# Kernel optimization log

Hardware: AMD Instinct MI355X
Metric: run time of the kernel (lower is better)

## Reference

```python
import jax, jax.numpy as jnp
import numpy as np

B, N, D, Z, H = 256, 128, 256, 64, 128

def setup_inputs() -> dict:
    key = jax.random.key(0)
    ks = jax.random.split(key, 12)
    s = 0.02
    inp = {
        "h_obs": jax.random.normal(ks[0], (B, N, D), jnp.float32),
        "z": jax.random.normal(ks[1], (B, N, Z), jnp.float32),
        "start_pos": jax.random.normal(ks[2], (B, N, 2), jnp.float32),
        # input_proj: Linear(D+Z+2 -> H)
        "W_in": jax.random.normal(ks[3], (D + Z + 2, H), jnp.float32) * s,
        "b_in": jax.random.normal(ks[4], (H,), jnp.float32) * s,
        # GRUCell weights, PyTorch layout: [3H, H] rows ordered (r, z, n)
        "W_ih": jax.random.normal(ks[5], (3 * H, H), jnp.float32) * s,
        "b_ih": jax.random.normal(ks[6], (3 * H,), jnp.float32) * s,
        "W_hh": jax.random.normal(ks[7], (3 * H, H), jnp.float32) * s,
        "b_hh": jax.random.normal(ks[8], (3 * H,), jnp.float32) * s,
        # out_proj: Linear(H -> 2)
        "W_out": jax.random.normal(ks[9], (2, H), jnp.float32) * s,
        "b_out": jax.random.normal(ks[10], (2,), jnp.float32) * s,
        "pred_len": 30,
    }
    return inp

def _gru_cell(x, h, W_ih, b_ih, W_hh, b_hh):
    gi = x @ W_ih.T + b_ih            # [BN, 3H]
    gh = h @ W_hh.T + b_hh            # [BN, 3H]
    i_r, i_z, i_n = jnp.split(gi, 3, axis=-1)
    h_r, h_z, h_n = jnp.split(gh, 3, axis=-1)
    r = jax.nn.sigmoid(i_r + h_r)
    zg = jax.nn.sigmoid(i_z + h_z)
    n = jnp.tanh(i_n + r * h_n)
    return (1.0 - zg) * n + zg * h

def reference(h_obs, z, start_pos, W_in, b_in, W_ih, b_ih, W_hh, b_hh, W_out, b_out, pred_len):
    BN = B * N
    # h_obs and z are constant across steps: precompute their projection once.
    base = jnp.concatenate([h_obs, z], axis=-1).reshape(BN, D + Z)
    base_proj = base @ W_in[: D + Z] + b_in            # [BN, H]
    W_pos = W_in[D + Z:]                               # [2, H]

    state0 = jnp.zeros((BN, H), h_obs.dtype)
    pos0 = start_pos.reshape(BN, 2)

    def step(carry, _):
        state, pos = carry
        x = base_proj + pos @ W_pos                    # == input_proj(cat(h,z,pos))
        state = _gru_cell(x, state, W_ih, b_ih, W_hh, b_hh)
        delta = state @ W_out.T + b_out                # [BN, 2]
        pos = pos + delta
        return (state, pos), pos

    (_, _), traj = jax.lax.scan(step, (state0, pos0), None, length=pred_len)
    # traj: [T, BN, 2] -> [B, T, N, 2]
    return traj.reshape(pred_len, B, N, 2).transpose(1, 0, 2, 3)
```

## Files before the change

kernel.cpp:

```cpp
#include <hip/hip_runtime.h>
#include <hip/hip_bf16.h>


#define T_LEN 30
#define H_    128
#define G3_   384
#define KIN_  320
#define S_    152
#define HBYTES (64*S_*2)
#define TRAJ_OFF (2*HBYTES)
#define LDS_BYTES (TRAJ_OFF + T_LEN*64*2*4)

#define SCL_RZ -1.44269504088896341f
#define SCL_N   2.88539008177792681f

typedef float  f32x4 __attribute__((ext_vector_type(4)));
typedef __bf16 b16x8 __attribute__((ext_vector_type(8)));

#define MFMA16(a,b,c) __builtin_amdgcn_mfma_f32_16x16x32_bf16((a),(b),(c),0,0,0)

__device__ __forceinline__ b16x8 pack8s(const float* p, float s){
  b16x8 r;
  #pragma unroll
  for (int i=0;i<8;i++) r[i] = (__bf16)(s*p[i]);
  return r;
}

__global__ void prep_wc(const float* __restrict__ W_in, const float* __restrict__ W_ih,
                        __bf16* __restrict__ WcT){
  __shared__ float win[H_];
  int k = blockIdx.x;
  if (threadIdx.x < H_) win[threadIdx.x] = W_in[(size_t)k*H_ + threadIdx.x];
  __syncthreads();
  int j = threadIdx.x;
  const float* wr = W_ih + (size_t)j*H_;
  float s = 0.f;
  #pragma unroll 8
  for (int m=0;m<H_;m++) s += wr[m]*win[m];
  float scl = (j < 2*H_) ? SCL_RZ : SCL_N;
  WcT[(size_t)j*KIN_ + k] = (__bf16)(scl*s);
}

__global__ void prep_vec(const float* __restrict__ W_in, const float* __restrict__ b_in,
                         const float* __restrict__ W_ih, const float* __restrict__ b_ih,
                         const float* __restrict__ b_hh,
                         float* __restrict__ cvec, float* __restrict__ P2G){
  int j = threadIdx.x;
  const float* wr = W_ih + (size_t)j*H_;
  float s  = b_ih[j] + (j < 2*H_ ? b_hh[j] : 0.f);
  float p0 = 0.f, p1 = 0.f;
  #pragma unroll 8
  for (int m=0;m<H_;m++){
    float w = wr[m];
    s  += b_in[m]*w;
    p0 += W_in[(size_t)KIN_*H_ + m]*w;
    p1 += W_in[(size_t)(KIN_+1)*H_ + m]*w;
  }
  float scl = (j < 2*H_) ? SCL_RZ : SCL_N;
  cvec[j] = scl*s; P2G[j] = scl*p0; P2G[G3_ + j] = scl*p1;
}

__global__ __launch_bounds__(512, 2)
void decoder(const float* __restrict__ h_obs, const float* __restrict__ zin,
             const float* __restrict__ start_pos,
             const float* __restrict__ W_hh, const float* __restrict__ b_hh,
             const float* __restrict__ W_out, const float* __restrict__ b_out,
             const __bf16* __restrict__ WcT, const float* __restrict__ cvec,
             const float* __restrict__ P2G, float* __restrict__ out)
{
  __shared__ __align__(16) char lds[LDS_BYTES];
  __bf16* hbuf = (__bf16*)lds;
  float*  traj = (float*)(lds + TRAJ_OFF);
  __bf16* stg  = (__bf16*)lds;

  const int tid  = threadIdx.x;
  const int lane = tid & 63;
  const int w    = tid >> 6;
  const int l15  = lane & 15;
  const int lhi  = lane >> 4;
  const int R0   = blockIdx.x << 6;
  const int hcol = (w<<4) + l15;
  const int jr = hcol, jz = H_ + hcol, jn = 2*H_ + hcol;
  const int oc = l15 & 1;

  {
    const float4* src = reinterpret_cast<const float4*>(h_obs) + (size_t)R0*64;
    #pragma unroll
    for (int i=0;i<8;i++){
      int k = tid + (i<<9);
      float4 v = src[k];
      int r = k>>6, c = (k&63)<<2;
      __bf16* d = &stg[r*328 + c];
      d[0]=(__bf16)v.x; d[1]=(__bf16)v.y; d[2]=(__bf16)v.z; d[3]=(__bf16)v.w;
    }
    const float4* srcz = reinterpret_cast<const float4*>(zin) + (size_t)R0*16;
    #pragma unroll
    for (int i=0;i<2;i++){
      int k = tid + (i<<9);
      float4 v = srcz[k];
      int r = k>>4, c = 256 + ((k&15)<<2);
      __bf16* d = &stg[r*328 + c];
      d[0]=(__bf16)v.x; d[1]=(__bf16)v.y; d[2]=(__bf16)v.z; d[3]=(__bf16)v.w;
    }
  }
  __syncthreads();

  f32x4 G[2][3][2];
  {
    float cr = cvec[jr], cz = cvec[jz], cn = cvec[jn];
    #pragma unroll
    for (int g=0; g<2; g++){
      G[g][0][0] = (f32x4){cr,cr,cr,cr}; G[g][0][1] = G[g][0][0];
      G[g][1][0] = (f32x4){cz,cz,cz,cz}; G[g][1][1] = G[g][1][0];
      G[g][2][0] = (f32x4){cn,cn,cn,cn}; G[g][2][1] = G[g][2][0];
    }
    #pragma unroll 1
    for (int kk=0; kk<10; kk++){
      const int ko = (kk<<5) + (lhi<<3);
      b16x8 br = *reinterpret_cast<const b16x8*>(WcT + (size_t)jr*KIN_ + ko);
      b16x8 bz = *reinterpret_cast<const b16x8*>(WcT + (size_t)jz*KIN_ + ko);
      b16x8 bn = *reinterpret_cast<const b16x8*>(WcT + (size_t)jn*KIN_ + ko);
      #pragma unroll
      for (int g=0; g<2; g++){
        b16x8 a0 = *reinterpret_cast<const b16x8*>(&stg[(g*32   +l15)*328 + ko]);
        b16x8 a1 = *reinterpret_cast<const b16x8*>(&stg[(g*32+16+l15)*328 + ko]);
        G[g][0][0] = MFMA16(a0, br, G[g][0][0]); G[g][0][1] = MFMA16(a1, br, G[g][0][1]);
        G[g][1][0] = MFMA16(a0, bz, G[g][1][0]); G[g][1][1] = MFMA16(a1, bz, G[g][1][1]);
        G[g][2][0] = MFMA16(a0, bn, G[g][2][0]); G[g][2][1] = MFMA16(a1, bn, G[g][2][1]);
      }
    }
  }

  b16x8 Bh[3][4], Bo[4];
  #pragma unroll
  for (int kk=0;kk<4;kk++){
    const int ko = (kk<<5) + (lhi<<3);
    Bh[0][kk] = pack8s(W_hh + (size_t)jr*H_ + ko, SCL_RZ);
    Bh[1][kk] = pack8s(W_hh + (size_t)jz*H_ + ko, SCL_RZ);
    Bh[2][kk] = pack8s(W_hh + (size_t)jn*H_ + ko, SCL_N);
    Bo[kk]    = pack8s(W_out + (size_t)oc*H_ + ko, 1.0f);
  }
  const float pgr0 = P2G[jr], pgr1 = P2G[G3_+jr];
  const float pgz0 = P2G[jz], pgz1 = P2G[G3_+jz];
  const float pgn0 = P2G[jn], pgn1 = P2G[G3_+jn];
  const float bhn  = SCL_N * b_hh[2*H_ + hcol];
  const float bo   = b_out[oc];
  const f32x4 bovec  = (f32x4){bo,bo,bo,bo};
  const f32x4 bhnvec = (f32x4){bhn,bhn,bhn,bhn};

  float posx[2][2][4], posy[2][2][4], st[2][2][4];
  #pragma unroll
  for (int g=0; g<2; g++)
    #pragma unroll
    for (int m=0;m<2;m++)
      #pragma unroll
      for (int q=0;q<4;q++){
        int r = R0 + (g<<5) + (m<<4) + (lhi<<2) + q;
        posx[g][m][q] = start_pos[2*r];
        posy[g][m][q] = start_pos[2*r+1];
      }

  __syncthreads();

  #pragma unroll
  for (int g=0; g<2; g++)
    #pragma unroll
    for (int m=0;m<2;m++)
      #pragma unroll
      for (int q=0;q<4;q++){
        float p0 = posx[g][m][q], p1 = posy[g][m][q];
        float rg = __builtin_amdgcn_rcpf(1.f + __builtin_amdgcn_exp2f(
                     fmaf(p1,pgr1, fmaf(p0,pgr0, G[g][0][m][q]))));
        float zg = __builtin_amdgcn_rcpf(1.f + __builtin_amdgcn_exp2f(
                     fmaf(p1,pgz1, fmaf(p0,pgz0, G[g][1][m][q]))));
        float inn = fmaf(p1,pgn1, fmaf(p0,pgn0, G[g][2][m][q]));
        float nn = fmaf(-2.f, __builtin_amdgcn_rcpf(1.f + __builtin_amdgcn_exp2f(
                     fmaf(rg, bhn, inn))), 1.f);
        float hnew = nn - zg*nn;
        st[g][m][q] = hnew;
        hbuf[((g<<5)+(m<<4)+(lhi<<2)+q)*S_ + hcol] = (__bf16)hnew;
      }

  const unsigned rdbA = (unsigned)(l15*(S_*2) + (lhi<<4));
  const unsigned wrbA = (unsigned)((lhi<<2)*(S_*2) + hcol*2);

  int cur = 0;
  #pragma unroll 1
  for (int t=1; t<T_LEN; ++t){
    __syncthreads();
    const char* rb = lds + cur*HBYTES;
    char*       wb = lds + (cur^1)*HBYTES;

    #pragma unroll
    for (int g=0; g<2; g++){
      const unsigned go = g*(32*S_*2);
      f32x4 ar0, ar1, az0, az1, an0, an1, d0, d1;
      #pragma unroll
      for (int kk=0;kk<4;kk++){
        b16x8 a0 = *reinterpret_cast<const b16x8*>(rb + go + rdbA + kk*64);
        b16x8 a1 = *reinterpret_cast<const b16x8*>(rb + go + rdbA + 16*S_*2 + kk*64);
        if (kk==0){
          d0  = MFMA16(a0, Bo[0],   bovec);  d1  = MFMA16(a1, Bo[0],   bovec);
          ar0 = MFMA16(a0, Bh[0][0], G[g][0][0]); ar1 = MFMA16(a1, Bh[0][0], G[g][0][1]);
          az0 = MFMA16(a0, Bh[1][0], G[g][1][0]); az1 = MFMA16(a1, Bh[1][0], G[g][1][1]);
          an0 = MFMA16(a0, Bh[2][0], bhnvec);     an1 = MFMA16(a1, Bh[2][0], bhnvec);
        } else {
          d0  = MFMA16(a0, Bo[kk],   d0);  d1  = MFMA16(a1, Bo[kk],   d1);
          ar0 = MFMA16(a0, Bh[0][kk], ar0); ar1 = MFMA16(a1, Bh[0][kk], ar1);
          az0 = MFMA16(a0, Bh[1][kk], az0); az1 = MFMA16(a1, Bh[1][kk], az1);
          an0 = MFMA16(a0, Bh[2][kk], an0); an1 = MFMA16(a1, Bh[2][kk], an1);
        }
      }
      #pragma unroll
      for (int m=0;m<2;m++)
        #pragma unroll
        for (int q=0;q<4;q++){
          float dme  = (m==0)? d0[q] : d1[q];
          float doth = __shfl_xor(dme, 1);
          posx[g][m][q] += oc ? doth : dme;
          posy[g][m][q] += oc ? dme  : doth;
        }
      if (w==g && l15==0){
        #pragma unroll
        for (int m=0;m<2;m++)
          #pragma unroll
          for (int q=0;q<4;q++){
            int rr = (g<<5) + (m<<4) + (lhi<<2) + q;
            float2 v; v.x = posx[g][m][q]; v.y = posy[g][m][q];
            *reinterpret_cast<float2*>(&traj[(t-1)*128 + rr*2]) = v;
          }
      }
      #pragma unroll
      for (int m=0;m<2;m++)
        #pragma unroll
        for (int q=0;q<4;q++){
          float p0 = posx[g][m][q], p1 = posy[g][m][q];
          float ar = (m==0)? ar0[q] : ar1[q];
          float az = (m==0)? az0[q] : az1[q];
          float hn = (m==0)? an0[q] : an1[q];
          float rg = __builtin_amdgcn_rcpf(1.f + __builtin_amdgcn_exp2f(
                       fmaf(p1,pgr1, fmaf(p0,pgr0, ar))));
          float zg = __builtin_amdgcn_rcpf(1.f + __builtin_amdgcn_exp2f(
                       fmaf(p1,pgz1, fmaf(p0,pgz0, az))));
          float inn = fmaf(p1,pgn1, fmaf(p0,pgn0, G[g][2][m][q]));
          float nn = fmaf(-2.f, __builtin_amdgcn_rcpf(1.f + __builtin_amdgcn_exp2f(
                       fmaf(rg, hn, inn))), 1.f);
          float hnew = fmaf(zg, st[g][m][q] - nn, nn);
          st[g][m][q] = hnew;
          *reinterpret_cast<__bf16*>(wb + go + wrbA + (m*16+q)*(S_*2)) = (__bf16)hnew;
        }
    }
    cur ^= 1;
  }

  __syncthreads();
  {
    const char* rb = lds + cur*HBYTES;
    #pragma unroll
    for (int g=0; g<2; g++){
      const unsigned go = g*(32*S_*2);
      f32x4 d0, d1;
      #pragma unroll
      for (int kk=0;kk<4;kk++){
        b16x8 a0 = *reinterpret_cast<const b16x8*>(rb + go + rdbA + kk*64);
        b16x8 a1 = *reinterpret_cast<const b16x8*>(rb + go + rdbA + 16*S_*2 + kk*64);
        if (kk==0){ d0 = MFMA16(a0, Bo[0], bovec); d1 = MFMA16(a1, Bo[0], bovec); }
        else      { d0 = MFMA16(a0, Bo[kk], d0);   d1 = MFMA16(a1, Bo[kk], d1);   }
      }
      #pragma unroll
      for (int m=0;m<2;m++)
        #pragma unroll
        for (int q=0;q<4;q++){
          float dme  = (m==0)? d0[q] : d1[q];
          float doth = __shfl_xor(dme, 1);
          posx[g][m][q] += oc ? doth : dme;
          posy[g][m][q] += oc ? dme  : doth;
        }
      if (w==g && l15==0){
        #pragma unroll
        for (int m=0;m<2;m++)
          #pragma unroll
          for (int q=0;q<4;q++){
            int rr = (g<<5) + (m<<4) + (lhi<<2) + q;
            float2 v; v.x = posx[g][m][q]; v.y = posy[g][m][q];
            *reinterpret_cast<float2*>(&traj[(T_LEN-1)*128 + rr*2]) = v;
          }
      }
    }
  }

  __syncthreads();
  {
    const size_t ob  = ((size_t)(R0>>7)*T_LEN)<<8;
    const int    n02 = (R0 & 127)<<1;
    for (int i=tid; i<T_LEN*128; i+=512){
      int tt = i>>7, j = i&127;
      out[ob + (size_t)tt*256 + n02 + j] = traj[i];
    }
  }
}

extern "C" void kernel_launch(void* const* d_in, const int* in_sizes, int n_in,
                              void* d_out, int out_size, void* d_ws, size_t ws_size,
                              hipStream_t stream) {
  const float* h_obs     = (const float*)d_in[0];
  const float* z         = (const float*)d_in[1];
  const float* start_pos = (const float*)d_in[2];
  const float* W_in      = (const float*)d_in[3];
  const float* b_in      = (const float*)d_in[4];
  const float* W_ih      = (const float*)d_in[5];
  const float* b_ih      = (const float*)d_in[6];
  const float* W_hh      = (const float*)d_in[7];
  const float* b_hh      = (const float*)d_in[8];
  const float* W_out     = (const float*)d_in[9];
  const float* b_out     = (const float*)d_in[10];

  __bf16* WcT  = (__bf16*)d_ws;
  float*  cvec = (float*)((char*)d_ws + (size_t)G3_*KIN_*2);
  float*  P2G  = cvec + G3_;

  prep_wc <<<KIN_, G3_, 0, stream>>>(W_in, W_ih, WcT);
  prep_vec<<<1,    G3_, 0, stream>>>(W_in, b_in, W_ih, b_ih, b_hh, cvec, P2G);
  decoder <<<512, 512, 0, stream>>>(h_obs, z, start_pos, W_hh, b_hh, W_out, b_out,
                                    WcT, cvec, P2G, (float*)d_out);
}
```

Before: 309.8 us.

## Fold position feedback into recurrent GEMM weights and pack input gates to bf16

Position feedback is folded algebraically into the recurrent weights: a prep kernel builds augmented weights in which pos@W_pos is rewritten through W_out applied to the previous hidden state, plus a small K-extension MFMA carrying the current position stored in LDS. This removes the per-element FMA position terms from the gate math. The precomputed input-gate accumulators are stored as packed bf16 to free registers. Only four designated waves compute the output delta instead of every wave, and prep_wc is re-tiled to 16 outputs per block. The trade-offs are extra MFMAs per step, lower precision from bf16 rounding of the gate inputs and positions, and an additional prep launch.

```diff
diff --git a/kernel.cpp b/kernel.cpp
--- a/kernel.cpp
+++ b/kernel.cpp
@@ -6,16 +6,17 @@
 #define H_    128
 #define G3_   384
 #define KIN_  320
-#define S_    152
-#define HBYTES (64*S_*2)
-#define TRAJ_OFF (2*HBYTES)
-#define LDS_BYTES (TRAJ_OFF + T_LEN*64*2*4)
+#define S2B   336
+#define HB    (64*S2B)
+#define TRAJ_OFF (2*HB)
+#define LDS_BYTES (TRAJ_OFF + T_LEN*64*8)
 
 #define SCL_RZ -1.44269504088896341f
 #define SCL_N   2.88539008177792681f
 
 typedef float  f32x4 __attribute__((ext_vector_type(4)));
 typedef __bf16 b16x8 __attribute__((ext_vector_type(8)));
+typedef unsigned u32x4 __attribute__((ext_vector_type(4)));
 
 #define MFMA16(a,b,c) __builtin_amdgcn_mfma_f32_16x16x32_bf16((a),(b),(c),0,0,0)
 
@@ -25,25 +26,52 @@
   for (int i=0;i<8;i++) r[i] = (__bf16)(s*p[i]);
   return r;
 }
+__device__ __forceinline__ unsigned pk2(float a, float b){
+  __bf16 x=(__bf16)a, y=(__bf16)b;
+  unsigned short ux=__builtin_bit_cast(unsigned short,x);
+  unsigned short uy=__builtin_bit_cast(unsigned short,y);
+  return (unsigned)ux | ((unsigned)uy<<16);
+}
+__device__ __forceinline__ f32x4 unpk2(unsigned lo, unsigned hi){
+  f32x4 r;
+  r[0]=__builtin_bit_cast(float, lo<<16);
+  r[1]=__builtin_bit_cast(float, lo&0xFFFF0000u);
+  r[2]=__builtin_bit_cast(float, hi<<16);
+  r[3]=__builtin_bit_cast(float, hi&0xFFFF0000u);
+  return r;
+}
+__device__ __forceinline__ b16x8 fragu(unsigned v){
+  u32x4 t = {v,0u,0u,0u};
+  return __builtin_bit_cast(b16x8, t);
+}
 
 __global__ void prep_wc(const float* __restrict__ W_in, const float* __restrict__ W_ih,
                         __bf16* __restrict__ WcT){
-  __shared__ float win[H_];
-  int k = blockIdx.x;
-  if (threadIdx.x < H_) win[threadIdx.x] = W_in[(size_t)k*H_ + threadIdx.x];
+  __shared__ float win[H_][16];
+  int k0 = blockIdx.x << 4;
+  for (int i=threadIdx.x; i<16*H_; i+=384){
+    int kk = i>>7, m = i&127;
+    win[m][kk] = W_in[(size_t)(k0+kk)*H_ + m];
+  }
   __syncthreads();
   int j = threadIdx.x;
   const float* wr = W_ih + (size_t)j*H_;
-  float s = 0.f;
-  #pragma unroll 8
-  for (int m=0;m<H_;m++) s += wr[m]*win[m];
+  float acc[16];
+  #pragma unroll
+  for (int kk=0;kk<16;kk++) acc[kk]=0.f;
+  for (int m=0;m<H_;m++){
+    float wv = wr[m];
+    #pragma unroll
+    for (int kk=0;kk<16;kk++) acc[kk] = fmaf(wv, win[m][kk], acc[kk]);
+  }
   float scl = (j < 2*H_) ? SCL_RZ : SCL_N;
-  WcT[(size_t)j*KIN_ + k] = (__bf16)(scl*s);
+  #pragma unroll
+  for (int kk=0;kk<16;kk++) WcT[(size_t)j*KIN_ + k0 + kk] = (__bf16)(scl*acc[kk]);
 }
 
 __global__ void prep_vec(const float* __restrict__ W_in, const float* __restrict__ b_in,
                          const float* __restrict__ W_ih, const float* __restrict__ b_ih,
-                         const float* __restrict__ b_hh,
+                         const float* __restrict__ b_hh, const float* __restrict__ b_out,
                          float* __restrict__ cvec, float* __restrict__ P2G){
   int j = threadIdx.x;
   const float* wr = W_ih + (size_t)j*H_;
@@ -51,27 +79,45 @@
   float p0 = 0.f, p1 = 0.f;
   #pragma unroll 8
   for (int m=0;m<H_;m++){
-    float w = wr[m];
-    s  += b_in[m]*w;
-    p0 += W_in[(size_t)KIN_*H_ + m]*w;
-    p1 += W_in[(size_t)(KIN_+1)*H_ + m]*w;
+    float wv = wr[m];
+    s  += b_in[m]*wv;
+    p0 += W_in[(size_t)KIN_*H_ + m]*wv;
+    p1 += W_in[(size_t)(KIN_+1)*H_ + m]*wv;
   }
   float scl = (j < 2*H_) ? SCL_RZ : SCL_N;
-  cvec[j] = scl*s; P2G[j] = scl*p0; P2G[G3_ + j] = scl*p1;
+  float p0s = scl*p0, p1s = scl*p1;
+  P2G[j] = p0s; P2G[G3_ + j] = p1s;
+  cvec[j] = scl*s + b_out[0]*p0s + b_out[1]*p1s;
+}
+
+__global__ void prep_wt(const float* __restrict__ W_hh, const float* __restrict__ W_out,
+                        const float* __restrict__ P2G, __bf16* __restrict__ WT){
+  int jp = blockIdx.x;
+  int set = jp >> 7, col = jp & 127;
+  int j = (set==0) ? col : (set==1) ? H_+col : 2*H_+col;
+  float p0 = P2G[j], p1 = P2G[G3_+j];
+  int k = threadIdx.x;
+  if (k >= 136) return;
+  float v = 0.f;
+  if (k < 128){
+    if (set<=1)      v = SCL_RZ*W_hh[(size_t)j*H_+k] + p0*W_out[k] + p1*W_out[H_+k];
+    else if (set==2) v = SCL_N *W_hh[(size_t)j*H_+k];
+    else             v = p0*W_out[k] + p1*W_out[H_+k];
+  } else if (k==128){ v = (set==2)? 0.f : p0; }
+  else if (k==129){ v = (set==2)? 0.f : p1; }
+  WT[(size_t)jp*136 + k] = (__bf16)v;
 }
 
 __global__ __launch_bounds__(512, 2)
 void decoder(const float* __restrict__ h_obs, const float* __restrict__ zin,
              const float* __restrict__ start_pos,
-             const float* __restrict__ W_hh, const float* __restrict__ b_hh,
-             const float* __restrict__ W_out, const float* __restrict__ b_out,
+             const float* __restrict__ b_hh, const float* __restrict__ W_out,
+             const float* __restrict__ b_out,
              const __bf16* __restrict__ WcT, const float* __restrict__ cvec,
-             const float* __restrict__ P2G, float* __restrict__ out)
+             const __bf16* __restrict__ WT, float* __restrict__ out)
 {
   __shared__ __align__(16) char lds[LDS_BYTES];
-  __bf16* hbuf = (__bf16*)lds;
-  float*  traj = (float*)(lds + TRAJ_OFF);
-  __bf16* stg  = (__bf16*)lds;
+  __bf16* stg = (__bf16*)lds;
 
   const int tid  = threadIdx.x;
   const int lane = tid & 63;
@@ -82,6 +128,8 @@
   const int hcol = (w<<4) + l15;
   const int jr = hcol, jz = H_ + hcol, jn = 2*H_ + hcol;
   const int oc = l15 & 1;
+  const bool desig = (w < 4);
+  const int gd = w >> 1, md = w & 1;
 
   {
     const float4* src = reinterpret_cast<const float4*>(h_obs) + (size_t)R0*64;
@@ -103,10 +151,41 @@
       d[0]=(__bf16)v.x; d[1]=(__bf16)v.y; d[2]=(__bf16)v.z; d[3]=(__bf16)v.w;
     }
   }
+
+  const float bo0 = b_out[0], bo1 = b_out[1];
+  const float bo  = oc ? bo1 : bo0;
+  const float bhn = SCL_N * b_hh[2*H_ + hcol];
+  const f32x4 bhnvec = (f32x4){bhn,bhn,bhn,bhn};
+
+  b16x8 Br[4],Bz[4],Ban[4],Binn[4],Bo[4];
+  #pragma unroll
+  for (int kk=0;kk<4;kk++){
+    const int ko = kk*32 + lhi*8;
+    Br[kk]   = *reinterpret_cast<const b16x8*>(WT + (size_t)(      hcol)*136 + ko);
+    Bz[kk]   = *reinterpret_cast<const b16x8*>(WT + (size_t)(128 + hcol)*136 + ko);
+    Ban[kk]  = *reinterpret_cast<const b16x8*>(WT + (size_t)(256 + hcol)*136 + ko);
+    Binn[kk] = *reinterpret_cast<const b16x8*>(WT + (size_t)(384 + hcol)*136 + ko);
+    Bo[kk]   = pack8s(W_out + (size_t)oc*H_ + ko, 1.0f);
+  }
+  const b16x8 Br4 = fragu(lhi==0 ? *reinterpret_cast<const unsigned*>(WT + (size_t)(      hcol)*136 + 128) : 0u);
+  const b16x8 Bz4 = fragu(lhi==0 ? *reinterpret_cast<const unsigned*>(WT + (size_t)(128 + hcol)*136 + 128) : 0u);
+  const b16x8 Bi4 = fragu(lhi==0 ? *reinterpret_cast<const unsigned*>(WT + (size_t)(384 + hcol)*136 + 128) : 0u);
+
+  float px[4]={0,0,0,0}, py[4]={0,0,0,0};
+  if (desig){
+    #pragma unroll
+    for (int q=0;q<4;q++){
+      int r = R0 + gd*32 + md*16 + lhi*4 + q;
+      px[q] = start_pos[2*r]   - bo0;
+      py[q] = start_pos[2*r+1] - bo1;
+    }
+  }
+
   __syncthreads();
 
-  f32x4 G[2][3][2];
+  unsigned Gp[2][3][2][2];
   {
+    f32x4 G[2][3][2];
     float cr = cvec[jr], cz = cvec[jz], cn = cvec[jn];
     #pragma unroll
     for (int g=0; g<2; g++){
@@ -129,168 +208,170 @@
         G[g][2][0] = MFMA16(a0, bn, G[g][2][0]); G[g][2][1] = MFMA16(a1, bn, G[g][2][1]);
       }
     }
-  }
-
-  b16x8 Bh[3][4], Bo[4];
+    #pragma unroll
+    for (int g=0; g<2; g++)
+      #pragma unroll
+      for (int gate=0; gate<3; gate++)
+        #pragma unroll
+        for (int m=0; m<2; m++){
+          Gp[g][gate][m][0] = pk2(G[g][gate][m][0], G[g][gate][m][1]);
+          Gp[g][gate][m][1] = pk2(G[g][gate][m][2], G[g][gate][m][3]);
+        }
+  }
+  __syncthreads();
+
+  for (int i=tid; i<4096; i+=512){
+    int r = i>>6, wq = i&63;
+    *reinterpret_cast<unsigned*>(lds + r*S2B + wq*4) = 0u;
+  }
+  if (desig && l15==0){
+    #pragma unroll
+    for (int q=0;q<4;q++){
+      int row = gd*32 + md*16 + lhi*4 + q;
+      *reinterpret_cast<unsigned*>(lds + row*S2B + 256) = pk2(px[q], py[q]);
+    }
+  }
+
+  float st[2][2][4];
   #pragma unroll
-  for (int kk=0;kk<4;kk++){
-    const int ko = (kk<<5) + (lhi<<3);
-    Bh[0][kk] = pack8s(W_hh + (size_t)jr*H_ + ko, SCL_RZ);
-    Bh[1][kk] = pack8s(W_hh + (size_t)jz*H_ + ko, SCL_RZ);
-    Bh[2][kk] = pack8s(W_hh + (size_t)jn*H_ + ko, SCL_N);
-    Bo[kk]    = pack8s(W_out + (size_t)oc*H_ + ko, 1.0f);
-  }
-  const float pgr0 = P2G[jr], pgr1 = P2G[G3_+jr];
-  const float pgz0 = P2G[jz], pgz1 = P2G[G3_+jz];
-  const float pgn0 = P2G[jn], pgn1 = P2G[G3_+jn];
-  const float bhn  = SCL_N * b_hh[2*H_ + hcol];
-  const float bo   = b_out[oc];
-  const f32x4 bovec  = (f32x4){bo,bo,bo,bo};
-  const f32x4 bhnvec = (f32x4){bhn,bhn,bhn,bhn};
-
-  float posx[2][2][4], posy[2][2][4], st[2][2][4];
-  #pragma unroll
-  for (int g=0; g<2; g++)
+  for (int g=0;g<2;g++)
     #pragma unroll
     for (int m=0;m<2;m++)
       #pragma unroll
-      for (int q=0;q<4;q++){
-        int r = R0 + (g<<5) + (m<<4) + (lhi<<2) + q;
-        posx[g][m][q] = start_pos[2*r];
-        posy[g][m][q] = start_pos[2*r+1];
-      }
-
-  __syncthreads();
-
-  #pragma unroll
-  for (int g=0; g<2; g++)
-    #pragma unroll
-    for (int m=0;m<2;m++)
-      #pragma unroll
-      for (int q=0;q<4;q++){
-        float p0 = posx[g][m][q], p1 = posy[g][m][q];
-        float rg = __builtin_amdgcn_rcpf(1.f + __builtin_amdgcn_exp2f(
-                     fmaf(p1,pgr1, fmaf(p0,pgr0, G[g][0][m][q]))));
-        float zg = __builtin_amdgcn_rcpf(1.f + __builtin_amdgcn_exp2f(
-                     fmaf(p1,pgz1, fmaf(p0,pgz0, G[g][1][m][q]))));
-        float inn = fmaf(p1,pgn1, fmaf(p0,pgn0, G[g][2][m][q]));
-        float nn = fmaf(-2.f, __builtin_amdgcn_rcpf(1.f + __builtin_amdgcn_exp2f(
-                     fmaf(rg, bhn, inn))), 1.f);
-        float hnew = nn - zg*nn;
-        st[g][m][q] = hnew;
-        hbuf[((g<<5)+(m<<4)+(lhi<<2)+q)*S_ + hcol] = (__bf16)hnew;
-      }
-
-  const unsigned rdbA = (unsigned)(l15*(S_*2) + (lhi<<4));
-  const unsigned wrbA = (unsigned)((lhi<<2)*(S_*2) + hcol*2);
+      for (int q=0;q<4;q++) st[g][m][q] = 0.f;
+
+  const unsigned rdb = (unsigned)(l15*S2B + lhi*16);
+  const f32x4 zero4 = (f32x4){0,0,0,0};
 
   int cur = 0;
   #pragma unroll 1
-  for (int t=1; t<T_LEN; ++t){
+  for (int t=0; t<T_LEN; ++t){
     __syncthreads();
-    const char* rb = lds + cur*HBYTES;
-    char*       wb = lds + (cur^1)*HBYTES;
-
-    #pragma unroll
-    for (int g=0; g<2; g++){
-      const unsigned go = g*(32*S_*2);
-      f32x4 ar0, ar1, az0, az1, an0, an1, d0, d1;
+    const char* rb = lds + cur*HB;
+    char*       wb = lds + (cur^1)*HB;
+
+    #pragma unroll
+    for (int g=0; g<2; ++g){
+      const char* rg_ = rb + g*(32*S2B);
+      char*       wg_ = wb + g*(32*S2B);
+
+      f32x4 ar0 = unpk2(Gp[g][0][0][0], Gp[g][0][0][1]);
+      f32x4 ar1 = unpk2(Gp[g][0][1][0], Gp[g][0][1][1]);
+      f32x4 az0 = unpk2(Gp[g][1][0][0], Gp[g][1][0][1]);
+      f32x4 az1 = unpk2(Gp[g][1][1][0], Gp[g][1][1][1]);
+      f32x4 ai0 = unpk2(Gp[g][2][0][0], Gp[g][2][0][1]);
+      f32x4 ai1 = unpk2(Gp[g][2][1][0], Gp[g][2][1][1]);
+      f32x4 an0 = bhnvec, an1 = bhnvec;
+
       #pragma unroll
       for (int kk=0;kk<4;kk++){
-        b16x8 a0 = *reinterpret_cast<const b16x8*>(rb + go + rdbA + kk*64);
-        b16x8 a1 = *reinterpret_cast<const b16x8*>(rb + go + rdbA + 16*S_*2 + kk*64);
-        if (kk==0){
-          d0  = MFMA16(a0, Bo[0],   bovec);  d1  = MFMA16(a1, Bo[0],   bovec);
-          ar0 = MFMA16(a0, Bh[0][0], G[g][0][0]); ar1 = MFMA16(a1, Bh[0][0], G[g][0][1]);
-          az0 = MFMA16(a0, Bh[1][0], G[g][1][0]); az1 = MFMA16(a1, Bh[1][0], G[g][1][1]);
-          an0 = MFMA16(a0, Bh[2][0], bhnvec);     an1 = MFMA16(a1, Bh[2][0], bhnvec);
+        b16x8 a0 = *reinterpret_cast<const b16x8*>(rg_ + rdb + kk*64);
+        b16x8 a1 = *reinterpret_cast<const b16x8*>(rg_ + rdb + 16*S2B + kk*64);
+        ar0 = MFMA16(a0,Br[kk],ar0);   ar1 = MFMA16(a1,Br[kk],ar1);
+        az0 = MFMA16(a0,Bz[kk],az0);   az1 = MFMA16(a1,Bz[kk],az1);
+        an0 = MFMA16(a0,Ban[kk],an0);  an1 = MFMA16(a1,Ban[kk],an1);
+        ai0 = MFMA16(a0,Binn[kk],ai0); ai1 = MFMA16(a1,Binn[kk],ai1);
+      }
+      {
+        unsigned pp0 = *reinterpret_cast<const unsigned*>(rg_ + l15*S2B + 256);
+        unsigned pp1 = *reinterpret_cast<const unsigned*>(rg_ + (16+l15)*S2B + 256);
+        b16x8 a40 = fragu(lhi==0 ? pp0 : 0u);
+        b16x8 a41 = fragu(lhi==0 ? pp1 : 0u);
+        ar0 = MFMA16(a40,Br4,ar0); ar1 = MFMA16(a41,Br4,ar1);
+        az0 = MFMA16(a40,Bz4,az0); az1 = MFMA16(a41,Bz4,az1);
+        ai0 = MFMA16(a40,Bi4,ai0); ai1 = MFMA16(a41,Bi4,ai1);
+      }
+
+      if (desig && gd == g){
+        f32x4 d;
+        if (md==0){
+          b16x8 f0 = *reinterpret_cast<const b16x8*>(rg_ + rdb);
+          d = MFMA16(f0,Bo[0],zero4);
+          #pragma unroll
+          for (int kk=1;kk<4;kk++){
+            b16x8 fk = *reinterpret_cast<const b16x8*>(rg_ + rdb + kk*64);
+            d = MFMA16(fk,Bo[kk],d);
+          }
         } else {
-          d0  = MFMA16(a0, Bo[kk],   d0);  d1  = MFMA16(a1, Bo[kk],   d1);
-          ar0 = MFMA16(a0, Bh[0][kk], ar0); ar1 = MFMA16(a1, Bh[0][kk], ar1);
-          az0 = MFMA16(a0, Bh[1][kk], az0); az1 = MFMA16(a1, Bh[1][kk], az1);
-          an0 = MFMA16(a0, Bh[2][kk], an0); an1 = MFMA16(a1, Bh[2][kk], an1);
+          b16x8 f0 = *reinterpret_cast<const b16x8*>(rg_ + rdb + 16*S2B);
+          d = MFMA16(f0,Bo[0],zero4);
+          #pragma unroll
+          for (int kk=1;kk<4;kk++){
+            b16x8 fk = *reinterpret_cast<const b16x8*>(rg_ + rdb + 16*S2B + kk*64);
+            d = MFMA16(fk,Bo[kk],d);
+          }
         }
-      }
-      #pragma unroll
-      for (int m=0;m<2;m++)
         #pragma unroll
         for (int q=0;q<4;q++){
-          float dme  = (m==0)? d0[q] : d1[q];
+          float dme  = d[q] + bo;
           float doth = __shfl_xor(dme, 1);
-          posx[g][m][q] += oc ? doth : dme;
-          posy[g][m][q] += oc ? dme  : doth;
+          px[q] += oc ? doth : dme;
+          py[q] += oc ? dme  : doth;
         }
-      if (w==g && l15==0){
-        #pragma unroll
-        for (int m=0;m<2;m++)
+        if (l15==0){
           #pragma unroll
           for (int q=0;q<4;q++){
-            int rr = (g<<5) + (m<<4) + (lhi<<2) + q;
-            float2 v; v.x = posx[g][m][q]; v.y = posy[g][m][q];
-            *reinterpret_cast<float2*>(&traj[(t-1)*128 + rr*2]) = v;
+            int row = md*16 + lhi*4 + q;
+            if (t > 0){
+              float2 v; v.x = px[q]; v.y = py[q];
+              *reinterpret_cast<float2*>(lds + TRAJ_OFF + ((t-1)*64 + g*32 + row)*8) = v;
+            }
+            *reinterpret_cast<unsigned*>(wg_ + row*S2B + 256) = pk2(px[q], py[q]);
           }
-      }
-      #pragma unroll
-      for (int m=0;m<2;m++)
+        }
+      }
+
+      #pragma unroll
+      for (int m=0;m<2;m++){
+        f32x4 Ar = m? ar1:ar0, Az = m? az1:az0, An = m? an1:an0, Ai = m? ai1:ai0;
         #pragma unroll
         for (int q=0;q<4;q++){
-          float p0 = posx[g][m][q], p1 = posy[g][m][q];
-          float ar = (m==0)? ar0[q] : ar1[q];
-          float az = (m==0)? az0[q] : az1[q];
-          float hn = (m==0)? an0[q] : an1[q];
-          float rg = __builtin_amdgcn_rcpf(1.f + __builtin_amdgcn_exp2f(
-                       fmaf(p1,pgr1, fmaf(p0,pgr0, ar))));
-          float zg = __builtin_amdgcn_rcpf(1.f + __builtin_amdgcn_exp2f(
-                       fmaf(p1,pgz1, fmaf(p0,pgz0, az))));
-          float inn = fmaf(p1,pgn1, fmaf(p0,pgn0, G[g][2][m][q]));
-          float nn = fmaf(-2.f, __builtin_amdgcn_rcpf(1.f + __builtin_amdgcn_exp2f(
-                       fmaf(rg, hn, inn))), 1.f);
-          float hnew = fmaf(zg, st[g][m][q] - nn, nn);
-          st[g][m][q] = hnew;
-          *reinterpret_cast<__bf16*>(wb + go + wrbA + (m*16+q)*(S_*2)) = (__bf16)hnew;
+          float rgt = __builtin_amdgcn_rcpf(1.f + __builtin_amdgcn_exp2f(Ar[q]));
+          float zgt = __builtin_amdgcn_rcpf(1.f + __builtin_amdgcn_exp2f(Az[q]));
+          float na  = fmaf(rgt, An[q], Ai[q]);
+          float nn  = fmaf(-2.f, __builtin_amdgcn_rcpf(1.f + __builtin_amdgcn_exp2f(na)), 1.f);
+          float h   = fmaf(zgt, st[g][m][q] - nn, nn);
+          st[g][m][q] = h;
+          *reinterpret_cast<__bf16*>(wg_ + (m*16+lhi*4+q)*S2B + hcol*2) = (__bf16)h;
         }
+      }
     }
     cur ^= 1;
+  }
+
+  __syncthreads();
+  if (desig){
+    const char* rg_ = lds + cur*HB + gd*(32*S2B);
+    f32x4 d;
+    {
+      b16x8 f0 = *reinterpret_cast<const b16x8*>(rg_ + (md*16+l15)*S2B + lhi*16);
+      d = MFMA16(f0,Bo[0],zero4);
+      #pragma unroll
+      for (int kk=1;kk<4;kk++){
+        b16x8 fk = *reinterpret_cast<const b16x8*>(rg_ + (md*16+l15)*S2B + lhi*16 + kk*64);
+        d = MFMA16(fk,Bo[kk],d);
+      }
+    }
+    #pragma unroll
+    for (int q=0;q<4;q++){
+      float dme  = d[q] + bo;
+      float doth = __shfl_xor(dme, 1);
+      px[q] += oc ? doth : dme;
+      py[q] += oc ? dme  : doth;
+    }
+    if (l15==0){
+      #pragma unroll
+      for (int q=0;q<4;q++){
+        int row = gd*32 + md*16 + lhi*4 + q;
+        float2 v; v.x = px[q]; v.y = py[q];
+        *reinterpret_cast<float2*>(lds + TRAJ_OFF + ((T_LEN-1)*64 + row)*8) = v;
+      }
+    }
   }
 
   __syncthreads();
   {
-    const char* rb = lds + cur*HBYTES;
-    #pragma unroll
-    for (int g=0; g<2; g++){
-      const unsigned go = g*(32*S_*2);
-      f32x4 d0, d1;
-      #pragma unroll
-      for (int kk=0;kk<4;kk++){
-        b16x8 a0 = *reinterpret_cast<const b16x8*>(rb + go + rdbA + kk*64);
-        b16x8 a1 = *reinterpret_cast<const b16x8*>(rb + go + rdbA + 16*S_*2 + kk*64);
-        if (kk==0){ d0 = MFMA16(a0, Bo[0], bovec); d1 = MFMA16(a1, Bo[0], bovec); }
-        else      { d0 = MFMA16(a0, Bo[kk], d0);   d1 = MFMA16(a1, Bo[kk], d1);   }
-      }
-      #pragma unroll
-      for (int m=0;m<2;m++)
-        #pragma unroll
-        for (int q=0;q<4;q++){
-          float dme  = (m==0)? d0[q] : d1[q];
-          float doth = __shfl_xor(dme, 1);
-          posx[g][m][q] += oc ? doth : dme;
-          posy[g][m][q] += oc ? dme  : doth;
-        }
-      if (w==g && l15==0){
-        #pragma unroll
-        for (int m=0;m<2;m++)
-          #pragma unroll
-          for (int q=0;q<4;q++){
-            int rr = (g<<5) + (m<<4) + (lhi<<2) + q;
-            float2 v; v.x = posx[g][m][q]; v.y = posy[g][m][q];
-            *reinterpret_cast<float2*>(&traj[(T_LEN-1)*128 + rr*2]) = v;
-          }
-      }
-    }
-  }
-
-  __syncthreads();
-  {
+    const float* traj = reinterpret_cast<const float*>(lds + TRAJ_OFF);
     const size_t ob  = ((size_t)(R0>>7)*T_LEN)<<8;
     const int    n02 = (R0 & 127)<<1;
     for (int i=tid; i<T_LEN*128; i+=512){
@@ -315,12 +396,15 @@
   const float* W_out     = (const float*)d_in[9];
   const float* b_out     = (const float*)d_in[10];
 
-  __bf16* WcT  = (__bf16*)d_ws;
-  float*  cvec = (float*)((char*)d_ws + (size_t)G3_*KIN_*2);
-  float*  P2G  = cvec + G3_;
-
-  prep_wc <<<KIN_, G3_, 0, stream>>>(W_in, W_ih, WcT);
-  prep_vec<<<1,    G3_, 0, stream>>>(W_in, b_in, W_ih, b_ih, b_hh, cvec, P2G);
-  decoder <<<512, 512, 0, stream>>>(h_obs, z, start_pos, W_hh, b_hh, W_out, b_out,
-                                    WcT, cvec, P2G, (float*)d_out);
-}
+  char* ws = (char*)d_ws;
+  __bf16* WcT  = (__bf16*)ws;
+  float*  cvec = (float*)(ws + 245760);
+  float*  P2G  = (float*)(ws + 247296);
+  __bf16* WT   = (__bf16*)(ws + 250368);
+
+  prep_wc <<<20,  384, 0, stream>>>(W_in, W_ih, WcT);
+  prep_vec<<<1,   384, 0, stream>>>(W_in, b_in, W_ih, b_ih, b_hh, b_out, cvec, P2G);
+  prep_wt <<<512, 192, 0, stream>>>(W_hh, W_out, P2G, WT);
+  decoder <<<512, 512, 0, stream>>>(h_obs, z, start_pos, b_hh, W_out, b_out,
+                                    WcT, cvec, WT, (float*)d_out);
+}
```

Result: slower. 324.3 us (+4.7%).
